# Optimization experiments

Measured on AMD Instinct MI355X. Metric: run time of the kernel, lower is better.

Reference implementation:

```python
import jax, jax.numpy as jnp
import numpy as np

N = 50000   # nodes
E = 800000  # edges (avg degree 16)
F_IN, F_HID, F_OUT = 4, 64, 1


def setup_inputs() -> dict:
    key = jax.random.key(0)
    k1, k2, k3, k4 = jax.random.split(key, 4)
    x = jax.random.normal(k1, (N, F_IN), dtype=jnp.float32)
    edge_index = jax.random.randint(k2, (2, E), 0, N, dtype=jnp.int64)
    W1 = jax.random.normal(k3, (F_IN, F_HID), dtype=jnp.float32) * (1.0 / np.sqrt(F_IN))
    b1 = jnp.zeros((F_HID,), dtype=jnp.float32)
    W2 = jax.random.normal(k4, (F_HID, F_OUT), dtype=jnp.float32) * (1.0 / np.sqrt(F_HID))
    b2 = jnp.zeros((F_OUT,), dtype=jnp.float32)
    return {"x": x, "edge_index": edge_index, "W1": W1, "b1": b1, "W2": W2, "b2": b2}


def _gcn_conv(h, W, b, src, dst, norm, n_nodes):
    # h: [N, F_in] -> linear -> gather src -> scale by norm -> scatter-add at dst
    m = (h @ W)[src] * norm[:, None]          # [E+N, F_out]
    out = jax.ops.segment_sum(m, dst, num_segments=n_nodes)
    return out + b


def reference(x, edge_index, W1, b1, W2, b2):
    n = x.shape[0]
    loops = jnp.arange(n, dtype=edge_index.dtype)
    src = jnp.concatenate([edge_index[0], loops])  # add self loops (PyG default)
    dst = jnp.concatenate([edge_index[1], loops])
    # symmetric normalization: deg computed at target (col) as in PyG gcn_norm
    deg = jax.ops.segment_sum(jnp.ones_like(dst, dtype=x.dtype), dst, num_segments=n)
    dis = jnp.where(deg > 0, deg ** -0.5, 0.0)
    norm = dis[src] * dis[dst]                      # [E+N]

    h = jax.nn.relu(_gcn_conv(x, W1, b1, src, dst, norm, n))
    # F.dropout with training=False (inference) is identity
    out = _gcn_conv(h, W2, b2, src, dst, norm, n)
    return jax.nn.sigmoid(out)                      # [N, 1]
```

## Files before the change

### kernel.cpp

```cpp
#include <hip/hip_runtime.h>


#define FH 64
#define NPB 64
#define MAXBK 1024
#define CHB 4096
#define BCAP 2048

__global__ void k_fill(const int* __restrict__ src, const int* __restrict__ dst,
                       int* __restrict__ bcnt, unsigned int* __restrict__ ebuf,
                       int E, int nbk) {
    __shared__ int h[MAXBK];
    __shared__ int resv[MAXBK];
    int t = threadIdx.x;
    for (int i = t; i < nbk; i += 256) h[i] = 0;
    __syncthreads();
    int base = blockIdx.x * CHB;
    int end = min(base + CHB, E);
    for (int e = base + t; e < end; e += 256)
        atomicAdd(&h[dst[e] >> 6], 1);
    __syncthreads();
    for (int i = t; i < nbk; i += 256) {
        int c = h[i];
        resv[i] = c ? atomicAdd(&bcnt[i], c) : 0;
        h[i] = 0;
    }
    __syncthreads();
    for (int e = base + t; e < end; e += 256) {
        int d = dst[e];
        int b = d >> 6;
        int idx = resv[b] + atomicAdd(&h[b], 1);
        if (idx < BCAP)
            ebuf[(size_t)b * BCAP + idx] = ((unsigned)d << 16) | (unsigned)src[e];
    }
}

__global__ void k_finish1(const unsigned int* __restrict__ ebuf,
                          const int* __restrict__ bcnt,
                          const float* __restrict__ x,
                          float* __restrict__ dis, float* __restrict__ xd, int N) {
    __shared__ int lc[NPB];
    int b = blockIdx.x, t = threadIdx.x;
    if (t < NPB) lc[t] = 0;
    __syncthreads();
    int c = min(bcnt[b], BCAP);
    const unsigned int* eb = ebuf + (size_t)b * BCAP;
    for (int j = t; j < c; j += 256)
        atomicAdd(&lc[(eb[j] >> 16) & (NPB - 1)], 1);
    __syncthreads();
    int node = b * NPB + t;
    if (t < NPB && node < N) {
        float dn = rsqrtf((float)(lc[t] + 1));
        dis[node] = dn;
        float4 xv = *reinterpret_cast<const float4*>(x + (size_t)node * 4);
        float4 o;
        o.x = dn * xv.x; o.y = dn * xv.y; o.z = dn * xv.z; o.w = dn * xv.w;
        *reinterpret_cast<float4*>(xd + (size_t)node * 4) = o;
    }
}

__global__ void k_finish2(const unsigned int* __restrict__ ebuf,
                          const int* __restrict__ bcnt,
                          const float* __restrict__ xd, const float* __restrict__ dis,
                          const float* __restrict__ W1, const float* __restrict__ b1,
                          const float* __restrict__ W2, float* __restrict__ q, int N) {
    __shared__ float y4[NPB * 5];
    __shared__ float sW[4 * FH];
    __shared__ float sb1[FH];
    __shared__ float sW2[FH];
    int b = blockIdx.x, t = threadIdx.x;
    sW[t] = W1[t];
    if (t < FH) { sb1[t] = b1[t]; sW2[t] = W2[t]; }
    for (int i = t; i < NPB * 5; i += 256) y4[i] = 0.0f;
    __syncthreads();
    int c = min(bcnt[b], BCAP);
    const unsigned int* eb = ebuf + (size_t)b * BCAP;
    for (int j = t; j < c; j += 256) {
        unsigned int pe = eb[j];
        int local = (pe >> 16) & (NPB - 1);
        int s = pe & 0xffff;
        float4 xv = *reinterpret_cast<const float4*>(xd + (size_t)s * 4);
        atomicAdd(&y4[local * 5 + 0], xv.x);
        atomicAdd(&y4[local * 5 + 1], xv.y);
        atomicAdd(&y4[local * 5 + 2], xv.z);
        atomicAdd(&y4[local * 5 + 3], xv.w);
    }
    __syncthreads();
    int node = b * NPB + t;
    if (t < NPB && node < N) {
        float dn = dis[node];
        float4 xv = *reinterpret_cast<const float4*>(xd + (size_t)node * 4);
        float u0 = dn * (y4[t * 5 + 0] + xv.x);
        float u1 = dn * (y4[t * 5 + 1] + xv.y);
        float u2 = dn * (y4[t * 5 + 2] + xv.z);
        float u3 = dn * (y4[t * 5 + 3] + xv.w);
        float acc = 0.0f;
        #pragma unroll 8
        for (int f = 0; f < FH; ++f) {
            float hh = u0 * sW[f] + u1 * sW[FH + f] + u2 * sW[2 * FH + f] + u3 * sW[3 * FH + f] + sb1[f];
            hh = fmaxf(hh, 0.0f);
            acc += hh * sW2[f];
        }
        q[node] = acc * dn;
    }
}

__global__ void k_layer2(const unsigned int* __restrict__ ebuf,
                         const int* __restrict__ bcnt,
                         const float* __restrict__ q, const float* __restrict__ dis,
                         const float* __restrict__ b2, float* __restrict__ out, int N) {
    __shared__ float qt[NPB];
    __shared__ float sb2;
    int b = blockIdx.x, t = threadIdx.x;
    if (t == 0) sb2 = b2[0];
    if (t < NPB) qt[t] = 0.0f;
    __syncthreads();
    int c = min(bcnt[b], BCAP);
    const unsigned int* eb = ebuf + (size_t)b * BCAP;
    for (int j = t; j < c; j += 256) {
        unsigned int pe = eb[j];
        atomicAdd(&qt[(pe >> 16) & (NPB - 1)], q[pe & 0xffff]);
    }
    __syncthreads();
    int node = b * NPB + t;
    if (t < NPB && node < N) {
        float v = dis[node] * (q[node] + qt[t]) + sb2;
        out[node] = 1.0f / (1.0f + __expf(-v));
    }
}

extern "C" void kernel_launch(void* const* d_in, const int* in_sizes, int n_in,
                              void* d_out, int out_size, void* d_ws, size_t ws_size,
                              hipStream_t stream) {
    const float* x   = (const float*)d_in[0];
    const int*   ei  = (const int*)d_in[1];
    const float* W1  = (const float*)d_in[2];
    const float* b1  = (const float*)d_in[3];
    const float* W2  = (const float*)d_in[4];
    const float* b2  = (const float*)d_in[5];
    float* out = (float*)d_out;

    int N = in_sizes[0] / 4;
    int E = in_sizes[1] / 2;
    const int* src = ei;
    const int* dst = ei + E;
    int nbk = (N + NPB - 1) / NPB;
    int nbe = (E + CHB - 1) / CHB;

    char* ws = (char*)d_ws;
    size_t off = 0;
    auto alloc = [&](size_t bytes) {
        void* p = ws + off;
        off = (off + bytes + 255) & ~(size_t)255;
        return p;
    };
    float*        dis  = (float*)alloc((size_t)N * 4);
    float*        xd   = (float*)alloc((size_t)N * 16);
    float*        q    = (float*)alloc((size_t)N * 4);
    int*          bcnt = (int*)alloc((size_t)MAXBK * 4);
    unsigned int* ebuf = (unsigned int*)alloc((size_t)nbk * BCAP * 4);
    (void)ws_size;

    hipMemsetAsync(bcnt, 0, (size_t)MAXBK * 4, stream);

    k_fill<<<nbe, 256, 0, stream>>>(src, dst, bcnt, ebuf, E, nbk);
    k_finish1<<<nbk, 256, 0, stream>>>(ebuf, bcnt, x, dis, xd, N);
    k_finish2<<<nbk, 256, 0, stream>>>(ebuf, bcnt, xd, dis, W1, b1, W2, q, N);
    k_layer2<<<nbk, 256, 0, stream>>>(ebuf, bcnt, q, dis, b2, out, N);
}
```

Measured before the change: 125.0 us.

## Fold degree histogram into bucket-fill kernel and drop separate normalization pass

Extra blocks are added to the fill kernel that build a global per-node in-degree count with atomics, so the degree pass that re-read the edge buckets is removed. The aggregation and output kernels now compute rsqrt(deg+1) on the fly from that count instead of reading precomputed dis/xd arrays, which removes one kernel launch and the xd intermediate. In exchange there are global atomics on an N-sized counter and an extra cnt gather per edge in the aggregation loop. A single memset now clears both the counters and bcnt.

```diff
diff --git a/kernel.cpp b/kernel.cpp
--- a/kernel.cpp
+++ b/kernel.cpp
@@ -6,64 +6,46 @@
 #define MAXBK 1024
 #define CHB 4096
 #define BCAP 2048
+#define HIST_BLKS 1024
 
-__global__ void k_fill(const int* __restrict__ src, const int* __restrict__ dst,
-                       int* __restrict__ bcnt, unsigned int* __restrict__ ebuf,
-                       int E, int nbk) {
-    __shared__ int h[MAXBK];
-    __shared__ int resv[MAXBK];
+__global__ void k_fill_hist(const int* __restrict__ src, const int* __restrict__ dst,
+                            int* __restrict__ bcnt, int* __restrict__ cnt,
+                            unsigned int* __restrict__ ebuf, int E, int nbk, int nbe) {
     int t = threadIdx.x;
-    for (int i = t; i < nbk; i += 256) h[i] = 0;
-    __syncthreads();
-    int base = blockIdx.x * CHB;
-    int end = min(base + CHB, E);
-    for (int e = base + t; e < end; e += 256)
-        atomicAdd(&h[dst[e] >> 6], 1);
-    __syncthreads();
-    for (int i = t; i < nbk; i += 256) {
-        int c = h[i];
-        resv[i] = c ? atomicAdd(&bcnt[i], c) : 0;
-        h[i] = 0;
-    }
-    __syncthreads();
-    for (int e = base + t; e < end; e += 256) {
-        int d = dst[e];
-        int b = d >> 6;
-        int idx = resv[b] + atomicAdd(&h[b], 1);
-        if (idx < BCAP)
-            ebuf[(size_t)b * BCAP + idx] = ((unsigned)d << 16) | (unsigned)src[e];
+    if ((int)blockIdx.x < nbe) {
+        __shared__ int h[MAXBK];
+        __shared__ int resv[MAXBK];
+        for (int i = t; i < nbk; i += 256) h[i] = 0;
+        __syncthreads();
+        int base = blockIdx.x * CHB;
+        int end = min(base + CHB, E);
+        for (int e = base + t; e < end; e += 256)
+            atomicAdd(&h[dst[e] >> 6], 1);
+        __syncthreads();
+        for (int i = t; i < nbk; i += 256) {
+            int c = h[i];
+            resv[i] = c ? atomicAdd(&bcnt[i], c) : 0;
+            h[i] = 0;
+        }
+        __syncthreads();
+        for (int e = base + t; e < end; e += 256) {
+            int d = dst[e];
+            int b = d >> 6;
+            int idx = resv[b] + atomicAdd(&h[b], 1);
+            if (idx < BCAP)
+                ebuf[(size_t)b * BCAP + idx] = ((unsigned)d << 16) | (unsigned)src[e];
+        }
+    } else {
+        for (int e = ((int)blockIdx.x - nbe) * 256 + t; e < E; e += HIST_BLKS * 256)
+            atomicAdd(&cnt[dst[e]], 1);
     }
 }
 
-__global__ void k_finish1(const unsigned int* __restrict__ ebuf,
-                          const int* __restrict__ bcnt,
-                          const float* __restrict__ x,
-                          float* __restrict__ dis, float* __restrict__ xd, int N) {
-    __shared__ int lc[NPB];
-    int b = blockIdx.x, t = threadIdx.x;
-    if (t < NPB) lc[t] = 0;
-    __syncthreads();
-    int c = min(bcnt[b], BCAP);
-    const unsigned int* eb = ebuf + (size_t)b * BCAP;
-    for (int j = t; j < c; j += 256)
-        atomicAdd(&lc[(eb[j] >> 16) & (NPB - 1)], 1);
-    __syncthreads();
-    int node = b * NPB + t;
-    if (t < NPB && node < N) {
-        float dn = rsqrtf((float)(lc[t] + 1));
-        dis[node] = dn;
-        float4 xv = *reinterpret_cast<const float4*>(x + (size_t)node * 4);
-        float4 o;
-        o.x = dn * xv.x; o.y = dn * xv.y; o.z = dn * xv.z; o.w = dn * xv.w;
-        *reinterpret_cast<float4*>(xd + (size_t)node * 4) = o;
-    }
-}
-
-__global__ void k_finish2(const unsigned int* __restrict__ ebuf,
-                          const int* __restrict__ bcnt,
-                          const float* __restrict__ xd, const float* __restrict__ dis,
-                          const float* __restrict__ W1, const float* __restrict__ b1,
-                          const float* __restrict__ W2, float* __restrict__ q, int N) {
+__global__ void k_agg(const unsigned int* __restrict__ ebuf,
+                      const int* __restrict__ bcnt, const int* __restrict__ cnt,
+                      const float* __restrict__ x,
+                      const float* __restrict__ W1, const float* __restrict__ b1,
+                      const float* __restrict__ W2, float* __restrict__ q, int N) {
     __shared__ float y4[NPB * 5];
     __shared__ float sW[4 * FH];
     __shared__ float sb1[FH];
@@ -79,21 +61,22 @@
         unsigned int pe = eb[j];
         int local = (pe >> 16) & (NPB - 1);
         int s = pe & 0xffff;
-        float4 xv = *reinterpret_cast<const float4*>(xd + (size_t)s * 4);
-        atomicAdd(&y4[local * 5 + 0], xv.x);
-        atomicAdd(&y4[local * 5 + 1], xv.y);
-        atomicAdd(&y4[local * 5 + 2], xv.z);
-        atomicAdd(&y4[local * 5 + 3], xv.w);
+        float4 xv = *reinterpret_cast<const float4*>(x + (size_t)s * 4);
+        float w = rsqrtf((float)(cnt[s] + 1));
+        atomicAdd(&y4[local * 5 + 0], w * xv.x);
+        atomicAdd(&y4[local * 5 + 1], w * xv.y);
+        atomicAdd(&y4[local * 5 + 2], w * xv.z);
+        atomicAdd(&y4[local * 5 + 3], w * xv.w);
     }
     __syncthreads();
     int node = b * NPB + t;
     if (t < NPB && node < N) {
-        float dn = dis[node];
-        float4 xv = *reinterpret_cast<const float4*>(xd + (size_t)node * 4);
-        float u0 = dn * (y4[t * 5 + 0] + xv.x);
-        float u1 = dn * (y4[t * 5 + 1] + xv.y);
-        float u2 = dn * (y4[t * 5 + 2] + xv.z);
-        float u3 = dn * (y4[t * 5 + 3] + xv.w);
+        float dn = rsqrtf((float)(cnt[node] + 1));
+        float4 xv = *reinterpret_cast<const float4*>(x + (size_t)node * 4);
+        float u0 = dn * (y4[t * 5 + 0] + dn * xv.x);
+        float u1 = dn * (y4[t * 5 + 1] + dn * xv.y);
+        float u2 = dn * (y4[t * 5 + 2] + dn * xv.z);
+        float u3 = dn * (y4[t * 5 + 3] + dn * xv.w);
         float acc = 0.0f;
         #pragma unroll 8
         for (int f = 0; f < FH; ++f) {
@@ -106,9 +89,9 @@
 }
 
 __global__ void k_layer2(const unsigned int* __restrict__ ebuf,
-                         const int* __restrict__ bcnt,
-                         const float* __restrict__ q, const float* __restrict__ dis,
-                         const float* __restrict__ b2, float* __restrict__ out, int N) {
+                         const int* __restrict__ bcnt, const int* __restrict__ cnt,
+                         const float* __restrict__ q, const float* __restrict__ b2,
+                         float* __restrict__ out, int N) {
     __shared__ float qt[NPB];
     __shared__ float sb2;
     int b = blockIdx.x, t = threadIdx.x;
@@ -124,7 +107,8 @@
     __syncthreads();
     int node = b * NPB + t;
     if (t < NPB && node < N) {
-        float v = dis[node] * (q[node] + qt[t]) + sb2;
+        float dn = rsqrtf((float)(cnt[node] + 1));
+        float v = dn * (q[node] + qt[t]) + sb2;
         out[node] = 1.0f / (1.0f + __expf(-v));
     }
 }
@@ -154,17 +138,17 @@
         off = (off + bytes + 255) & ~(size_t)255;
         return p;
     };
-    float*        dis  = (float*)alloc((size_t)N * 4);
-    float*        xd   = (float*)alloc((size_t)N * 16);
+    int*          cnt  = (int*)alloc((size_t)N * 4);
+    int*          bcnt = (int*)alloc((size_t)MAXBK * 4);
+    size_t        zlen = off;
     float*        q    = (float*)alloc((size_t)N * 4);
-    int*          bcnt = (int*)alloc((size_t)MAXBK * 4);
     unsigned int* ebuf = (unsigned int*)alloc((size_t)nbk * BCAP * 4);
     (void)ws_size;
 
-    hipMemsetAsync(bcnt, 0, (size_t)MAXBK * 4, stream);
+    hipMemsetAsync(ws, 0, zlen, stream);
 
-    k_fill<<<nbe, 256, 0, stream>>>(src, dst, bcnt, ebuf, E, nbk);
-    k_finish1<<<nbk, 256, 0, stream>>>(ebuf, bcnt, x, dis, xd, N);
-    k_finish2<<<nbk, 256, 0, stream>>>(ebuf, bcnt, xd, dis, W1, b1, W2, q, N);
-    k_layer2<<<nbk, 256, 0, stream>>>(ebuf, bcnt, q, dis, b2, out, N);
+    k_fill_hist<<<nbe + HIST_BLKS, 256, 0, stream>>>(src, dst, bcnt, cnt, ebuf,
+                                                     E, nbk, nbe);
+    k_agg<<<nbk, 256, 0, stream>>>(ebuf, bcnt, cnt, x, W1, b1, W2, q, N);
+    k_layer2<<<nbk, 256, 0, stream>>>(ebuf, bcnt, cnt, q, b2, out, N);
 }
```

After: 152.6 us. 1.22x slower.

## Coarsen edge buckets to 256 nodes and register-cache edges in fill

Applied to the files above, without the earlier changes.

The edge-binning pass now groups edges into coarse buckets of 256 destination nodes, and each fill block handles 8192 edges held in registers (32 per thread), so dst/src are read once instead of twice. There are fewer buckets and fewer global reservation atomics. The downstream kernels launch four blocks per coarse bucket, and each scans the whole bucket but keeps only its 64-node quarter. That means every edge entry is read four times per pass, and BCAP of 8192 per 256-node bucket leaves less headroom against overflow.

```diff
diff --git a/kernel.cpp b/kernel.cpp
--- a/kernel.cpp
+++ b/kernel.cpp
@@ -2,54 +2,69 @@
 
 
 #define FH 64
-#define NPB 64
-#define MAXBK 1024
-#define CHB 4096
-#define BCAP 2048
+#define NPC 256
+#define NBC_MAX 256
+#define CHB 8192
+#define EPT 32
+#define BCAP 8192
+#define NPF 64
 
 __global__ void k_fill(const int* __restrict__ src, const int* __restrict__ dst,
                        int* __restrict__ bcnt, unsigned int* __restrict__ ebuf,
-                       int E, int nbk) {
-    __shared__ int h[MAXBK];
-    __shared__ int resv[MAXBK];
+                       int E, int nbc) {
+    __shared__ int h[NBC_MAX];
+    __shared__ int resv[NBC_MAX];
     int t = threadIdx.x;
-    for (int i = t; i < nbk; i += 256) h[i] = 0;
+    if (t < nbc) h[t] = 0;
     __syncthreads();
     int base = blockIdx.x * CHB;
-    int end = min(base + CHB, E);
-    for (int e = base + t; e < end; e += 256)
-        atomicAdd(&h[dst[e] >> 6], 1);
-    __syncthreads();
-    for (int i = t; i < nbk; i += 256) {
-        int c = h[i];
-        resv[i] = c ? atomicAdd(&bcnt[i], c) : 0;
-        h[i] = 0;
+    unsigned int pe[EPT];
+    #pragma unroll
+    for (int k = 0; k < EPT; ++k) {
+        int e = base + k * 256 + t;
+        if (e < E) {
+            int d = dst[e];
+            pe[k] = ((unsigned)d << 16) | (unsigned)src[e];
+            atomicAdd(&h[d >> 8], 1);
+        } else {
+            pe[k] = 0xffffffffu;
+        }
     }
     __syncthreads();
-    for (int e = base + t; e < end; e += 256) {
-        int d = dst[e];
-        int b = d >> 6;
-        int idx = resv[b] + atomicAdd(&h[b], 1);
-        if (idx < BCAP)
-            ebuf[(size_t)b * BCAP + idx] = ((unsigned)d << 16) | (unsigned)src[e];
+    if (t < nbc) {
+        int c = h[t];
+        resv[t] = c ? atomicAdd(&bcnt[t], c) : 0;
+        h[t] = 0;
+    }
+    __syncthreads();
+    #pragma unroll
+    for (int k = 0; k < EPT; ++k) {
+        if (pe[k] != 0xffffffffu) {
+            int b = pe[k] >> 24;
+            int idx = resv[b] + atomicAdd(&h[b], 1);
+            if (idx < BCAP) ebuf[(size_t)b * BCAP + idx] = pe[k];
+        }
     }
 }
 
 __global__ void k_finish1(const unsigned int* __restrict__ ebuf,
                           const int* __restrict__ bcnt,
-                          const float* __restrict__ x,
-                          float* __restrict__ dis, float* __restrict__ xd, int N) {
-    __shared__ int lc[NPB];
-    int b = blockIdx.x, t = threadIdx.x;
-    if (t < NPB) lc[t] = 0;
+                          const float* __restrict__ x, float* __restrict__ dis,
+                          float* __restrict__ xd, int N) {
+    __shared__ int lc[NPF];
+    int f = blockIdx.x, t = threadIdx.x;
+    int cb = f >> 2, w = f & 3;
+    if (t < NPF) lc[t] = 0;
     __syncthreads();
-    int c = min(bcnt[b], BCAP);
-    const unsigned int* eb = ebuf + (size_t)b * BCAP;
-    for (int j = t; j < c; j += 256)
-        atomicAdd(&lc[(eb[j] >> 16) & (NPB - 1)], 1);
+    int c = min(bcnt[cb], BCAP);
+    const unsigned int* eb = ebuf + (size_t)cb * BCAP;
+    for (int j = t; j < c; j += 256) {
+        int local = (eb[j] >> 16) & 255;
+        if ((local >> 6) == w) atomicAdd(&lc[local & 63], 1);
+    }
     __syncthreads();
-    int node = b * NPB + t;
-    if (t < NPB && node < N) {
+    int node = f * NPF + t;
+    if (t < NPF && node < N) {
         float dn = rsqrtf((float)(lc[t] + 1));
         dis[node] = dn;
         float4 xv = *reinterpret_cast<const float4*>(x + (size_t)node * 4);
@@ -59,35 +74,40 @@
     }
 }
 
-__global__ void k_finish2(const unsigned int* __restrict__ ebuf,
-                          const int* __restrict__ bcnt,
-                          const float* __restrict__ xd, const float* __restrict__ dis,
-                          const float* __restrict__ W1, const float* __restrict__ b1,
-                          const float* __restrict__ W2, float* __restrict__ q, int N) {
-    __shared__ float y4[NPB * 5];
+__global__ void k_agg(const unsigned int* __restrict__ ebuf,
+                      const int* __restrict__ bcnt,
+                      const float* __restrict__ xd, const float* __restrict__ dis,
+                      const float* __restrict__ W1, const float* __restrict__ b1,
+                      const float* __restrict__ W2, float* __restrict__ q, int N) {
+    __shared__ float y4[NPF * 5];
     __shared__ float sW[4 * FH];
     __shared__ float sb1[FH];
     __shared__ float sW2[FH];
-    int b = blockIdx.x, t = threadIdx.x;
+    int f = blockIdx.x, t = threadIdx.x;
+    int cb = f >> 2, w = f & 3;
     sW[t] = W1[t];
     if (t < FH) { sb1[t] = b1[t]; sW2[t] = W2[t]; }
-    for (int i = t; i < NPB * 5; i += 256) y4[i] = 0.0f;
+    if (t < NPF * 5) y4[t] = 0.0f;
+    if (t + 256 < NPF * 5) y4[t + 256] = 0.0f;
     __syncthreads();
-    int c = min(bcnt[b], BCAP);
-    const unsigned int* eb = ebuf + (size_t)b * BCAP;
+    int c = min(bcnt[cb], BCAP);
+    const unsigned int* eb = ebuf + (size_t)cb * BCAP;
     for (int j = t; j < c; j += 256) {
         unsigned int pe = eb[j];
-        int local = (pe >> 16) & (NPB - 1);
-        int s = pe & 0xffff;
-        float4 xv = *reinterpret_cast<const float4*>(xd + (size_t)s * 4);
-        atomicAdd(&y4[local * 5 + 0], xv.x);
-        atomicAdd(&y4[local * 5 + 1], xv.y);
-        atomicAdd(&y4[local * 5 + 2], xv.z);
-        atomicAdd(&y4[local * 5 + 3], xv.w);
+        int local = (pe >> 16) & 255;
+        if ((local >> 6) == w) {
+            int s = pe & 0xffff;
+            float4 xv = *reinterpret_cast<const float4*>(xd + (size_t)s * 4);
+            int l = local & 63;
+            atomicAdd(&y4[l * 5 + 0], xv.x);
+            atomicAdd(&y4[l * 5 + 1], xv.y);
+            atomicAdd(&y4[l * 5 + 2], xv.z);
+            atomicAdd(&y4[l * 5 + 3], xv.w);
+        }
     }
     __syncthreads();
-    int node = b * NPB + t;
-    if (t < NPB && node < N) {
+    int node = f * NPF + t;
+    if (t < NPF && node < N) {
         float dn = dis[node];
         float4 xv = *reinterpret_cast<const float4*>(xd + (size_t)node * 4);
         float u0 = dn * (y4[t * 5 + 0] + xv.x);
@@ -96,10 +116,10 @@
         float u3 = dn * (y4[t * 5 + 3] + xv.w);
         float acc = 0.0f;
         #pragma unroll 8
-        for (int f = 0; f < FH; ++f) {
-            float hh = u0 * sW[f] + u1 * sW[FH + f] + u2 * sW[2 * FH + f] + u3 * sW[3 * FH + f] + sb1[f];
+        for (int ff = 0; ff < FH; ++ff) {
+            float hh = u0 * sW[ff] + u1 * sW[FH + ff] + u2 * sW[2 * FH + ff] + u3 * sW[3 * FH + ff] + sb1[ff];
             hh = fmaxf(hh, 0.0f);
-            acc += hh * sW2[f];
+            acc += hh * sW2[ff];
         }
         q[node] = acc * dn;
     }
@@ -109,21 +129,24 @@
                          const int* __restrict__ bcnt,
                          const float* __restrict__ q, const float* __restrict__ dis,
                          const float* __restrict__ b2, float* __restrict__ out, int N) {
-    __shared__ float qt[NPB];
+    __shared__ float qt[NPF];
     __shared__ float sb2;
-    int b = blockIdx.x, t = threadIdx.x;
+    int f = blockIdx.x, t = threadIdx.x;
+    int cb = f >> 2, w = f & 3;
     if (t == 0) sb2 = b2[0];
-    if (t < NPB) qt[t] = 0.0f;
+    if (t < NPF) qt[t] = 0.0f;
     __syncthreads();
-    int c = min(bcnt[b], BCAP);
-    const unsigned int* eb = ebuf + (size_t)b * BCAP;
+    int c = min(bcnt[cb], BCAP);
+    const unsigned int* eb = ebuf + (size_t)cb * BCAP;
     for (int j = t; j < c; j += 256) {
         unsigned int pe = eb[j];
-        atomicAdd(&qt[(pe >> 16) & (NPB - 1)], q[pe & 0xffff]);
+        int local = (pe >> 16) & 255;
+        if ((local >> 6) == w)
+            atomicAdd(&qt[local & 63], q[pe & 0xffff]);
     }
     __syncthreads();
-    int node = b * NPB + t;
-    if (t < NPB && node < N) {
+    int node = f * NPF + t;
+    if (t < NPF && node < N) {
         float v = dis[node] * (q[node] + qt[t]) + sb2;
         out[node] = 1.0f / (1.0f + __expf(-v));
     }
@@ -144,8 +167,9 @@
     int E = in_sizes[1] / 2;
     const int* src = ei;
     const int* dst = ei + E;
-    int nbk = (N + NPB - 1) / NPB;
+    int nbc = (N + NPC - 1) / NPC;
     int nbe = (E + CHB - 1) / CHB;
+    int nbf = nbc * 4;
 
     char* ws = (char*)d_ws;
     size_t off = 0;
@@ -157,14 +181,14 @@
     float*        dis  = (float*)alloc((size_t)N * 4);
     float*        xd   = (float*)alloc((size_t)N * 16);
     float*        q    = (float*)alloc((size_t)N * 4);
-    int*          bcnt = (int*)alloc((size_t)MAXBK * 4);
-    unsigned int* ebuf = (unsigned int*)alloc((size_t)nbk * BCAP * 4);
+    int*          bcnt = (int*)alloc((size_t)NBC_MAX * 4);
+    unsigned int* ebuf = (unsigned int*)alloc((size_t)nbc * BCAP * 4);
     (void)ws_size;
 
-    hipMemsetAsync(bcnt, 0, (size_t)MAXBK * 4, stream);
+    hipMemsetAsync(bcnt, 0, (size_t)NBC_MAX * 4, stream);
 
-    k_fill<<<nbe, 256, 0, stream>>>(src, dst, bcnt, ebuf, E, nbk);
-    k_finish1<<<nbk, 256, 0, stream>>>(ebuf, bcnt, x, dis, xd, N);
-    k_finish2<<<nbk, 256, 0, stream>>>(ebuf, bcnt, xd, dis, W1, b1, W2, q, N);
-    k_layer2<<<nbk, 256, 0, stream>>>(ebuf, bcnt, q, dis, b2, out, N);
+    k_fill<<<nbe, 256, 0, stream>>>(src, dst, bcnt, ebuf, E, nbc);
+    k_finish1<<<nbf, 256, 0, stream>>>(ebuf, bcnt, x, dis, xd, N);
+    k_agg<<<nbf, 256, 0, stream>>>(ebuf, bcnt, xd, dis, W1, b1, W2, q, N);
+    k_layer2<<<nbf, 256, 0, stream>>>(ebuf, bcnt, q, dis, b2, out, N);
 }
```

New measurement: 129.9 us. +3.9%, slower.

## Replace global-atomic bucket fill with per-chunk sub-buckets compacted in finish pass

Applied to the files above, without the earlier changes.

The fill kernel makes a single pass: each edge chunk writes into its own fixed-size sub-bucket slot for each coarse 256-node bucket, so there is no global atomic reservation and no second histogram pass. k_finish1 then compacts the sub-buckets into contiguous per-bucket lists using a prefix over chunk counts, while also computing degrees. Buckets grow from 64 to 256 nodes and chunks from 4096 to 8192 edges, so there are fewer, larger blocks. The price is an extra read and write of the edge list during compaction. Edges are silently dropped if a sub-bucket overflows its SUB=96 entries, which relies on the uniform random degree distribution.

```diff
diff --git a/kernel.cpp b/kernel.cpp
--- a/kernel.cpp
+++ b/kernel.cpp
@@ -2,54 +2,66 @@
 
 
 #define FH 64
-#define NPB 64
-#define MAXBK 1024
-#define CHB 4096
-#define BCAP 2048
+#define NPC 256
+#define NBC_MAX 256
+#define CHB 8192
+#define SUB 96
+#define NFB_MAX 128
+#define BCAP2 5120
 
 __global__ void k_fill(const int* __restrict__ src, const int* __restrict__ dst,
-                       int* __restrict__ bcnt, unsigned int* __restrict__ ebuf,
-                       int E, int nbk) {
-    __shared__ int h[MAXBK];
-    __shared__ int resv[MAXBK];
-    int t = threadIdx.x;
-    for (int i = t; i < nbk; i += 256) h[i] = 0;
+                       int* __restrict__ gcnt, unsigned int* __restrict__ ebuf,
+                       int E, int nbc, int nfb) {
+    __shared__ int h[NBC_MAX];
+    int t = threadIdx.x, blk = blockIdx.x;
+    if (t < nbc) h[t] = 0;
     __syncthreads();
-    int base = blockIdx.x * CHB;
-    int end = min(base + CHB, E);
-    for (int e = base + t; e < end; e += 256)
-        atomicAdd(&h[dst[e] >> 6], 1);
-    __syncthreads();
-    for (int i = t; i < nbk; i += 256) {
-        int c = h[i];
-        resv[i] = c ? atomicAdd(&bcnt[i], c) : 0;
-        h[i] = 0;
+    int base = blk * CHB, end = min(base + CHB, E);
+    for (int e = base + t; e < end; e += 256) {
+        int d = dst[e];
+        int b = d >> 8;
+        int pos = atomicAdd(&h[b], 1);
+        if (pos < SUB)
+            ebuf[((size_t)b * nfb + blk) * SUB + pos] = ((unsigned)d << 16) | (unsigned)src[e];
     }
     __syncthreads();
-    for (int e = base + t; e < end; e += 256) {
-        int d = dst[e];
-        int b = d >> 6;
-        int idx = resv[b] + atomicAdd(&h[b], 1);
-        if (idx < BCAP)
-            ebuf[(size_t)b * BCAP + idx] = ((unsigned)d << 16) | (unsigned)src[e];
-    }
+    if (t < nbc) gcnt[(size_t)blk * nbc + t] = min(h[t], SUB);
 }
 
 __global__ void k_finish1(const unsigned int* __restrict__ ebuf,
-                          const int* __restrict__ bcnt,
+                          const int* __restrict__ gcnt,
                           const float* __restrict__ x,
-                          float* __restrict__ dis, float* __restrict__ xd, int N) {
-    __shared__ int lc[NPB];
-    int b = blockIdx.x, t = threadIdx.x;
-    if (t < NPB) lc[t] = 0;
+                          float* __restrict__ dis, float* __restrict__ xd,
+                          unsigned int* __restrict__ ebuf2, int* __restrict__ ecnt,
+                          int N, int nbc, int nfb) {
+    __shared__ int cg[NFB_MAX];
+    __shared__ int pfx[NFB_MAX];
+    __shared__ int lc[NPC];
+    int cb = blockIdx.x, t = threadIdx.x;
+    if (t < nfb) cg[t] = gcnt[(size_t)t * nbc + cb];
+    lc[t] = 0;
     __syncthreads();
-    int c = min(bcnt[b], BCAP);
-    const unsigned int* eb = ebuf + (size_t)b * BCAP;
-    for (int j = t; j < c; j += 256)
-        atomicAdd(&lc[(eb[j] >> 16) & (NPB - 1)], 1);
+    if (t == 0) {
+        int run = 0;
+        for (int i = 0; i < nfb; ++i) { pfx[i] = run; run += cg[i]; }
+        ecnt[cb] = min(run, BCAP2);
+    }
     __syncthreads();
-    int node = b * NPB + t;
-    if (t < NPB && node < N) {
+    int tot = nfb * SUB;
+    const unsigned int* eb = ebuf + (size_t)cb * nfb * SUB;
+    unsigned int* e2 = ebuf2 + (size_t)cb * BCAP2;
+    for (int j = t; j < tot; j += 256) {
+        int blk = j / SUB, pos = j - blk * SUB;
+        if (pos < cg[blk]) {
+            unsigned int pe = eb[j];
+            int gidx = pfx[blk] + pos;
+            if (gidx < BCAP2) e2[gidx] = pe;
+            atomicAdd(&lc[(pe >> 16) & (NPC - 1)], 1);
+        }
+    }
+    __syncthreads();
+    int node = cb * NPC + t;
+    if (node < N) {
         float dn = rsqrtf((float)(lc[t] + 1));
         dis[node] = dn;
         float4 xv = *reinterpret_cast<const float4*>(x + (size_t)node * 4);
@@ -59,35 +71,36 @@
     }
 }
 
-__global__ void k_finish2(const unsigned int* __restrict__ ebuf,
-                          const int* __restrict__ bcnt,
-                          const float* __restrict__ xd, const float* __restrict__ dis,
-                          const float* __restrict__ W1, const float* __restrict__ b1,
-                          const float* __restrict__ W2, float* __restrict__ q, int N) {
-    __shared__ float y4[NPB * 5];
+__global__ void k_agg(const unsigned int* __restrict__ ebuf2,
+                      const int* __restrict__ ecnt,
+                      const float* __restrict__ xd, const float* __restrict__ dis,
+                      const float* __restrict__ W1, const float* __restrict__ b1,
+                      const float* __restrict__ W2, float* __restrict__ q, int N) {
+    __shared__ float y4[NPC * 5];
     __shared__ float sW[4 * FH];
     __shared__ float sb1[FH];
     __shared__ float sW2[FH];
-    int b = blockIdx.x, t = threadIdx.x;
+    int cb = blockIdx.x, t = threadIdx.x;
     sW[t] = W1[t];
     if (t < FH) { sb1[t] = b1[t]; sW2[t] = W2[t]; }
-    for (int i = t; i < NPB * 5; i += 256) y4[i] = 0.0f;
+    #pragma unroll
+    for (int i = t; i < NPC * 5; i += 256) y4[i] = 0.0f;
     __syncthreads();
-    int c = min(bcnt[b], BCAP);
-    const unsigned int* eb = ebuf + (size_t)b * BCAP;
+    int c = ecnt[cb];
+    const unsigned int* e2 = ebuf2 + (size_t)cb * BCAP2;
     for (int j = t; j < c; j += 256) {
-        unsigned int pe = eb[j];
-        int local = (pe >> 16) & (NPB - 1);
+        unsigned int pe = e2[j];
         int s = pe & 0xffff;
+        int l = (pe >> 16) & (NPC - 1);
         float4 xv = *reinterpret_cast<const float4*>(xd + (size_t)s * 4);
-        atomicAdd(&y4[local * 5 + 0], xv.x);
-        atomicAdd(&y4[local * 5 + 1], xv.y);
-        atomicAdd(&y4[local * 5 + 2], xv.z);
-        atomicAdd(&y4[local * 5 + 3], xv.w);
+        atomicAdd(&y4[l * 5 + 0], xv.x);
+        atomicAdd(&y4[l * 5 + 1], xv.y);
+        atomicAdd(&y4[l * 5 + 2], xv.z);
+        atomicAdd(&y4[l * 5 + 3], xv.w);
     }
     __syncthreads();
-    int node = b * NPB + t;
-    if (t < NPB && node < N) {
+    int node = cb * NPC + t;
+    if (node < N) {
         float dn = dis[node];
         float4 xv = *reinterpret_cast<const float4*>(xd + (size_t)node * 4);
         float u0 = dn * (y4[t * 5 + 0] + xv.x);
@@ -105,25 +118,23 @@
     }
 }
 
-__global__ void k_layer2(const unsigned int* __restrict__ ebuf,
-                         const int* __restrict__ bcnt,
+__global__ void k_layer2(const unsigned int* __restrict__ ebuf2,
+                         const int* __restrict__ ecnt,
                          const float* __restrict__ q, const float* __restrict__ dis,
                          const float* __restrict__ b2, float* __restrict__ out, int N) {
-    __shared__ float qt[NPB];
+    __shared__ float qt[NPC];
     __shared__ float sb2;
-    int b = blockIdx.x, t = threadIdx.x;
+    int cb = blockIdx.x, t = threadIdx.x;
     if (t == 0) sb2 = b2[0];
-    if (t < NPB) qt[t] = 0.0f;
+    qt[t] = 0.0f;
     __syncthreads();
-    int c = min(bcnt[b], BCAP);
-    const unsigned int* eb = ebuf + (size_t)b * BCAP;
-    for (int j = t; j < c; j += 256) {
-        unsigned int pe = eb[j];
-        atomicAdd(&qt[(pe >> 16) & (NPB - 1)], q[pe & 0xffff]);
-    }
+    int c = ecnt[cb];
+    const unsigned int* e2 = ebuf2 + (size_t)cb * BCAP2;
+    for (int j = t; j < c; j += 256)
+        atomicAdd(&qt[(e2[j] >> 16) & (NPC - 1)], q[e2[j] & 0xffff]);
     __syncthreads();
-    int node = b * NPB + t;
-    if (t < NPB && node < N) {
+    int node = cb * NPC + t;
+    if (node < N) {
         float v = dis[node] * (q[node] + qt[t]) + sb2;
         out[node] = 1.0f / (1.0f + __expf(-v));
     }
@@ -144,8 +155,8 @@
     int E = in_sizes[1] / 2;
     const int* src = ei;
     const int* dst = ei + E;
-    int nbk = (N + NPB - 1) / NPB;
-    int nbe = (E + CHB - 1) / CHB;
+    int nbc = (N + NPC - 1) / NPC;
+    int nfb = (E + CHB - 1) / CHB;
 
     char* ws = (char*)d_ws;
     size_t off = 0;
@@ -154,17 +165,17 @@
         off = (off + bytes + 255) & ~(size_t)255;
         return p;
     };
-    float*        dis  = (float*)alloc((size_t)N * 4);
-    float*        xd   = (float*)alloc((size_t)N * 16);
-    float*        q    = (float*)alloc((size_t)N * 4);
-    int*          bcnt = (int*)alloc((size_t)MAXBK * 4);
-    unsigned int* ebuf = (unsigned int*)alloc((size_t)nbk * BCAP * 4);
+    float*        dis   = (float*)alloc((size_t)N * 4);
+    float*        xd    = (float*)alloc((size_t)N * 16);
+    float*        q     = (float*)alloc((size_t)N * 4);
+    int*          gcnt  = (int*)alloc((size_t)nfb * nbc * 4);
+    int*          ecnt  = (int*)alloc((size_t)nbc * 4);
+    unsigned int* ebuf  = (unsigned int*)alloc((size_t)nbc * nfb * SUB * 4);
+    unsigned int* ebuf2 = (unsigned int*)alloc((size_t)nbc * BCAP2 * 4);
     (void)ws_size;
 
-    hipMemsetAsync(bcnt, 0, (size_t)MAXBK * 4, stream);
-
-    k_fill<<<nbe, 256, 0, stream>>>(src, dst, bcnt, ebuf, E, nbk);
-    k_finish1<<<nbk, 256, 0, stream>>>(ebuf, bcnt, x, dis, xd, N);
-    k_finish2<<<nbk, 256, 0, stream>>>(ebuf, bcnt, xd, dis, W1, b1, W2, q, N);
-    k_layer2<<<nbk, 256, 0, stream>>>(ebuf, bcnt, q, dis, b2, out, N);
+    k_fill<<<nfb, 256, 0, stream>>>(src, dst, gcnt, ebuf, E, nbc, nfb);
+    k_finish1<<<nbc, 256, 0, stream>>>(ebuf, gcnt, x, dis, xd, ebuf2, ecnt, N, nbc, nfb);
+    k_agg<<<nbc, 256, 0, stream>>>(ebuf2, ecnt, xd, dis, W1, b1, W2, q, N);
+    k_layer2<<<nbc, 256, 0, stream>>>(ebuf2, ecnt, q, dis, b2, out, N);
 }
```

Measured after the change: 143.4 us. 14.7% more time.
